# Optimization experiments

Hardware: AMD Instinct MI355X
Metric: run time of the kernel (lower is better)

Reference implementation:

```python
import jax, jax.numpy as jnp
import numpy as np

NUM_GRAPHS = 4
INPUT_SIZE = 50000          # nodes per graph
BOTTLENECK = 64
FFN = 128
HIDDEN = [1, 8, 16]         # hidden_channels; convs go 16->8 then 8->1
E = 3200000                 # num edges (avg degree 16)
N = NUM_GRAPHS * INPUT_SIZE # total nodes = 200000


def setup_inputs() -> dict:
    key = jax.random.key(0)
    ks = jax.random.split(key, 12)
    d = {}
    d["x"] = jax.random.normal(ks[0], (NUM_GRAPHS, BOTTLENECK), dtype=jnp.float32)
    d["edge_index"] = jax.random.randint(ks[1], (2, E), 0, N, dtype=jnp.int64)
    d["edge_weight"] = jax.random.uniform(ks[2], (E,), dtype=jnp.float32)
    # learned params (stored as [in, out] so forward is x @ W + b)
    d["fc1_w"] = jax.random.normal(ks[3], (BOTTLENECK, FFN), dtype=jnp.float32) / np.sqrt(BOTTLENECK)
    d["fc1_b"] = jnp.zeros((FFN,), dtype=jnp.float32)
    d["fc2_w"] = jax.random.normal(ks[4], (FFN, INPUT_SIZE * HIDDEN[-1]), dtype=jnp.float32) / np.sqrt(FFN)
    d["fc2_b"] = jnp.zeros((INPUT_SIZE * HIDDEN[-1],), dtype=jnp.float32)
    d["conv0_w"] = jax.random.normal(ks[5], (HIDDEN[2], HIDDEN[1]), dtype=jnp.float32) / np.sqrt(HIDDEN[2])
    d["conv0_b"] = jnp.zeros((HIDDEN[1],), dtype=jnp.float32)
    d["conv1_w"] = jax.random.normal(ks[6], (HIDDEN[1], HIDDEN[0]), dtype=jnp.float32) / np.sqrt(HIDDEN[1])
    d["conv1_b"] = jnp.zeros((HIDDEN[0],), dtype=jnp.float32)
    d["num_graphs"] = NUM_GRAPHS
    return d


def _gcn_conv(x, row, col, ew, W, b, n_nodes):
    """PyG GCNConv: add self loops (weight 1), symmetric normalization,
    scatter-add of normalized source features, then linear weight + bias."""
    loop = jnp.arange(n_nodes, dtype=row.dtype)
    r = jnp.concatenate([row, loop])
    c = jnp.concatenate([col, loop])
    w = jnp.concatenate([ew, jnp.ones((n_nodes,), dtype=ew.dtype)])
    deg = jax.ops.segment_sum(w, c, num_segments=n_nodes)          # [N]
    dinv = jnp.where(deg > 0, jax.lax.rsqrt(deg), 0.0)
    norm = dinv[r] * w * dinv[c]                                    # [E+N]
    h = x @ W                                                       # [N, out]
    msg = h[r] * norm[:, None]                                      # gather + scale
    out = jax.ops.segment_sum(msg, c, num_segments=n_nodes)        # scatter-add
    return out + b


def reference(x, edge_index, edge_weight, fc1_w, fc1_b, fc2_w, fc2_b,
              conv0_w, conv0_b, conv1_w, conv1_b, num_graphs):
    act = jax.nn.elu
    row, col = edge_index[0], edge_index[1]
    n_nodes = num_graphs * INPUT_SIZE
    z = act(x @ fc1_w + fc1_b)                                     # [G, ffn]
    z = act(z @ fc2_w + fc2_b)                                     # [G, input_size*hidden[-1]]
    h = z.reshape(n_nodes, HIDDEN[-1])                             # [N, 16]
    out = _gcn_conv(h, row, col, edge_weight, conv0_w, conv0_b, n_nodes)  # 16->8
    out = act(out)                                                 # act except last layer
    out = _gcn_conv(out, row, col, edge_weight, conv1_w, conv1_b, n_nodes)  # 8->1
    return out
```

## Files before the change

kernel.cpp:

```cpp
#include <hip/hip_runtime.h>
#include <cstddef>

#define NGRAPH  4
#define NPG     50000
#define NNODES  200000
#define BNECK   64
#define FFN     128
#define COLS    800000
#define NEDGE   3200000
#define H2      16
#define H1      8
#define SCAN_B  512
#define NB      ((NNODES + SCAN_B - 1) / SCAN_B)

__device__ __forceinline__ float elu(float x) {
    return x > 0.f ? x : expm1f(x);
}

__global__ void k_fc1(const float* __restrict__ x, const float* __restrict__ w,
                      const float* __restrict__ b, float* __restrict__ z1) {
    int t = threadIdx.x;
    int g = t >> 7, j = t & 127;
    float acc = b[j];
    #pragma unroll 8
    for (int i = 0; i < BNECK; ++i)
        acc = fmaf(x[g * BNECK + i], w[i * FFN + j], acc);
    z1[t] = elu(acc);
}

__global__ void k_zero(int* __restrict__ p, int n) {
    int i = blockIdx.x * blockDim.x + threadIdx.x;
    if (i < n) p[i] = 0;
}

__global__ void k_hist(const int* __restrict__ col, int* __restrict__ cnt) {
    int e = blockIdx.x * blockDim.x + threadIdx.x;
    if (e < NEDGE) atomicAdd(&cnt[col[e]], 1);
}

__global__ void k_bsum(const int* __restrict__ cnt, int* __restrict__ bsum) {
    __shared__ int s[SCAN_B];
    int t = threadIdx.x;
    int i = blockIdx.x * SCAN_B + t;
    s[t] = (i < NNODES) ? cnt[i] : 0;
    __syncthreads();
    for (int st = SCAN_B / 2; st > 0; st >>= 1) {
        if (t < st) s[t] += s[t + st];
        __syncthreads();
    }
    if (t == 0) bsum[blockIdx.x] = s[0];
}

__global__ void k_btop(const int* __restrict__ bsum, int* __restrict__ bstart) {
    __shared__ int s[SCAN_B];
    int t = threadIdx.x;
    int v = (t < NB) ? bsum[t] : 0;
    s[t] = v;
    __syncthreads();
    for (int st = 1; st < SCAN_B; st <<= 1) {
        int x = (t >= st) ? s[t - st] : 0;
        __syncthreads();
        s[t] += x;
        __syncthreads();
    }
    if (t < NB) bstart[t] = s[t] - v;
}

__global__ void k_bscan(int* __restrict__ cnt, const int* __restrict__ bstart) {
    __shared__ int s[SCAN_B];
    int t = threadIdx.x;
    int i = blockIdx.x * SCAN_B + t;
    int v = (i < NNODES) ? cnt[i] : 0;
    s[t] = v;
    __syncthreads();
    for (int st = 1; st < SCAN_B; st <<= 1) {
        int x = (t >= st) ? s[t - st] : 0;
        __syncthreads();
        s[t] += x;
        __syncthreads();
    }
    if (i < NNODES) cnt[i] = bstart[blockIdx.x] + s[t] - v;
}

__global__ void k_place(const int* __restrict__ row, const int* __restrict__ col,
                        const float* __restrict__ ew,
                        int* __restrict__ offs, int2* __restrict__ csr) {
    int e = blockIdx.x * blockDim.x + threadIdx.x;
    if (e >= NEDGE) return;
    int c = col[e];
    int pos = atomicAdd(&offs[c], 1);
    int2 ent;
    ent.x = row[e];
    ent.y = __float_as_int(ew[e]);
    csr[pos] = ent;
}

__global__ void k_deg(const int* __restrict__ offs, const int2* __restrict__ csr,
                      float* __restrict__ dinv) {
    int n = blockIdx.x * blockDim.x + threadIdx.x;
    if (n >= NNODES) return;
    int s0 = n ? offs[n - 1] : 0;
    int e0 = offs[n];
    float d = 1.0f;
    for (int j = s0; j < e0; ++j) d += __int_as_float(csr[j].y);
    dinv[n] = rsqrtf(d);
}

__global__ __launch_bounds__(256) void k_fc2(
    const float* __restrict__ z1, const float* __restrict__ w2,
    const float* __restrict__ b2, const float* __restrict__ cw0,
    const float* __restrict__ dinv,
    float* __restrict__ hws, float* __restrict__ acc0)
{
    __shared__ float s_z1[NGRAPH * FFN];
    __shared__ float s_cw[H2 * H1];
    __shared__ float s_h[NGRAPH][1024];

    int t = threadIdx.x;
    for (int i = t; i < NGRAPH * FFN; i += 256) s_z1[i] = z1[i];
    if (t < H2 * H1) s_cw[t] = cw0[t];
    __syncthreads();

    int j0 = blockIdx.x * 1024;
    int jj = j0 + t * 4;
    if (jj < COLS) {
        float4 a0 = {0,0,0,0}, a1 = {0,0,0,0}, a2 = {0,0,0,0}, a3 = {0,0,0,0};
        #pragma unroll 4
        for (int i = 0; i < FFN; ++i) {
            const float4 wv = *reinterpret_cast<const float4*>(&w2[(size_t)i * COLS + jj]);
            float zg0 = s_z1[0 * FFN + i];
            float zg1 = s_z1[1 * FFN + i];
            float zg2 = s_z1[2 * FFN + i];
            float zg3 = s_z1[3 * FFN + i];
            a0.x = fmaf(zg0, wv.x, a0.x); a0.y = fmaf(zg0, wv.y, a0.y);
            a0.z = fmaf(zg0, wv.z, a0.z); a0.w = fmaf(zg0, wv.w, a0.w);
            a1.x = fmaf(zg1, wv.x, a1.x); a1.y = fmaf(zg1, wv.y, a1.y);
            a1.z = fmaf(zg1, wv.z, a1.z); a1.w = fmaf(zg1, wv.w, a1.w);
            a2.x = fmaf(zg2, wv.x, a2.x); a2.y = fmaf(zg2, wv.y, a2.y);
            a2.z = fmaf(zg2, wv.z, a2.z); a2.w = fmaf(zg2, wv.w, a2.w);
            a3.x = fmaf(zg3, wv.x, a3.x); a3.y = fmaf(zg3, wv.y, a3.y);
            a3.z = fmaf(zg3, wv.z, a3.z); a3.w = fmaf(zg3, wv.w, a3.w);
        }
        const float4 bv = *reinterpret_cast<const float4*>(&b2[jj]);
        s_h[0][t*4+0] = elu(a0.x + bv.x); s_h[0][t*4+1] = elu(a0.y + bv.y);
        s_h[0][t*4+2] = elu(a0.z + bv.z); s_h[0][t*4+3] = elu(a0.w + bv.w);
        s_h[1][t*4+0] = elu(a1.x + bv.x); s_h[1][t*4+1] = elu(a1.y + bv.y);
        s_h[1][t*4+2] = elu(a1.z + bv.z); s_h[1][t*4+3] = elu(a1.w + bv.w);
        s_h[2][t*4+0] = elu(a2.x + bv.x); s_h[2][t*4+1] = elu(a2.y + bv.y);
        s_h[2][t*4+2] = elu(a2.z + bv.z); s_h[2][t*4+3] = elu(a2.w + bv.w);
        s_h[3][t*4+0] = elu(a3.x + bv.x); s_h[3][t*4+1] = elu(a3.y + bv.y);
        s_h[3][t*4+2] = elu(a3.z + bv.z); s_h[3][t*4+3] = elu(a3.w + bv.w);
    }
    __syncthreads();

    int nbase = j0 >> 4;
    for (int o = t; o < NGRAPH * 64 * H1; o += 256) {
        int g  = o >> 9;
        int lo = o & 511;
        int nl = lo >> 3;
        int m  = lo & 7;
        int nloc = nbase + nl;
        if (nloc < NPG) {
            const float* hr = &s_h[g][nl * 16];
            float s = 0.f;
            #pragma unroll
            for (int k = 0; k < H2; ++k) s = fmaf(hr[k], s_cw[k * H1 + m], s);
            int node = g * NPG + nloc;
            float di = dinv[node];
            hws[node * H1 + m]  = s * di;
            acc0[node * H1 + m] = s * (di * di);
        }
    }
}

__global__ void k_gather0(const int* __restrict__ offs, const int2* __restrict__ csr,
                          const float* __restrict__ hws, const float* __restrict__ acc0,
                          const float* __restrict__ b0, const float* __restrict__ cw1,
                          const float* __restrict__ dinv, float* __restrict__ h1s) {
    int n = blockIdx.x * blockDim.x + threadIdx.x;
    if (n >= NNODES) return;
    int s0 = n ? offs[n - 1] : 0;
    int e0 = offs[n];
    float4 mA = {0,0,0,0}, mB = {0,0,0,0};
    for (int j = s0; j < e0; ++j) {
        int2 ent = csr[j];
        int   r = ent.x;
        float w = __int_as_float(ent.y);
        const float4 ha = *reinterpret_cast<const float4*>(&hws[r * H1]);
        const float4 hb = *reinterpret_cast<const float4*>(&hws[r * H1 + 4]);
        mA.x = fmaf(ha.x, w, mA.x); mA.y = fmaf(ha.y, w, mA.y);
        mA.z = fmaf(ha.z, w, mA.z); mA.w = fmaf(ha.w, w, mA.w);
        mB.x = fmaf(hb.x, w, mB.x); mB.y = fmaf(hb.y, w, mB.y);
        mB.z = fmaf(hb.z, w, mB.z); mB.w = fmaf(hb.w, w, mB.w);
    }
    float dc = dinv[n];
    const float4 sA = *reinterpret_cast<const float4*>(&acc0[n * H1]);
    const float4 sB = *reinterpret_cast<const float4*>(&acc0[n * H1 + 4]);
    float s = 0.f;
    s = fmaf(elu(sA.x + dc * mA.x + b0[0]), cw1[0], s);
    s = fmaf(elu(sA.y + dc * mA.y + b0[1]), cw1[1], s);
    s = fmaf(elu(sA.z + dc * mA.z + b0[2]), cw1[2], s);
    s = fmaf(elu(sA.w + dc * mA.w + b0[3]), cw1[3], s);
    s = fmaf(elu(sB.x + dc * mB.x + b0[4]), cw1[4], s);
    s = fmaf(elu(sB.y + dc * mB.y + b0[5]), cw1[5], s);
    s = fmaf(elu(sB.z + dc * mB.z + b0[6]), cw1[6], s);
    s = fmaf(elu(sB.w + dc * mB.w + b0[7]), cw1[7], s);
    h1s[n] = s * dc;
}

__global__ void k_gather1(const int* __restrict__ offs, const int2* __restrict__ csr,
                          const float* __restrict__ h1s, const float* __restrict__ dinv,
                          const float* __restrict__ cb1, float* __restrict__ out) {
    int n = blockIdx.x * blockDim.x + threadIdx.x;
    if (n >= NNODES) return;
    int s0 = n ? offs[n - 1] : 0;
    int e0 = offs[n];
    float a = h1s[n];
    for (int j = s0; j < e0; ++j) {
        int2 ent = csr[j];
        a = fmaf(h1s[ent.x], __int_as_float(ent.y), a);
    }
    out[n] = cb1[0] + a * dinv[n];
}

extern "C" void kernel_launch(void* const* d_in, const int* in_sizes, int n_in,
                              void* d_out, int out_size, void* d_ws, size_t ws_size,
                              hipStream_t stream) {
    const float* x    = (const float*)d_in[0];
    const int*   ei   = (const int*)d_in[1];
    const float* ew   = (const float*)d_in[2];
    const float* fc1w = (const float*)d_in[3];
    const float* fc1b = (const float*)d_in[4];
    const float* fc2w = (const float*)d_in[5];
    const float* fc2b = (const float*)d_in[6];
    const float* cw0  = (const float*)d_in[7];
    const float* cb0  = (const float*)d_in[8];
    const float* cw1  = (const float*)d_in[9];
    const float* cb1  = (const float*)d_in[10];
    float* out = (float*)d_out;

    float* ws    = (float*)d_ws;
    float* z1    = ws;
    float* dinv  = ws + 512;
    float* hws   = dinv + NNODES;
    float* acc0  = hws + (size_t)NNODES * H1;
    float* h1s   = acc0 + (size_t)NNODES * H1;
    int*   offs  = (int*)(h1s + NNODES);
    int*   bsum  = offs + NNODES;
    int*   bst   = bsum + SCAN_B;
    int2*  csr   = (int2*)(bst + SCAN_B);

    const int* row = ei;
    const int* col = ei + NEDGE;

    k_fc1 <<<1, 512, 0, stream>>>(x, fc1w, fc1b, z1);
    k_zero<<<(NNODES + 255) / 256, 256, 0, stream>>>(offs, NNODES);
    k_hist<<<(NEDGE + 255) / 256, 256, 0, stream>>>(col, offs);
    k_bsum<<<NB, SCAN_B, 0, stream>>>(offs, bsum);
    k_btop<<<1, SCAN_B, 0, stream>>>(bsum, bst);
    k_bscan<<<NB, SCAN_B, 0, stream>>>(offs, bst);
    k_place<<<(NEDGE + 255) / 256, 256, 0, stream>>>(row, col, ew, offs, csr);
    k_deg<<<(NNODES + 255) / 256, 256, 0, stream>>>(offs, csr, dinv);
    k_fc2<<<(COLS + 1023) / 1024, 256, 0, stream>>>(z1, fc2w, fc2b, cw0, dinv, hws, acc0);
    k_gather0<<<(NNODES + 255) / 256, 256, 0, stream>>>(offs, csr, hws, acc0, cb0, cw1, dinv, h1s);
    k_gather1<<<(NNODES + 255) / 256, 256, 0, stream>>>(offs, csr, h1s, dinv, cb1, out);
}
```

Baseline: 1.101 ms.

## Build padded ELL adjacency with overflow list instead of CSR via scan

Replaces the histogram + three-kernel prefix scan + CSR placement with a single ELL placement kernel that writes each edge into a fixed-width (40) per-node slot, spilling rare high-degree edges into a small overflow list. Placement blocks are partitioned by destination range to localize atomics, at the cost of rereading the edge list multiple times. Degree and both gather kernels are rewritten for the ELL layout with a linear scan of the overflow list for spilled nodes. The path is selected only if the workspace is large enough; otherwise the old CSR path is used.

```diff
diff --git a/kernel.cpp b/kernel.cpp
--- a/kernel.cpp
+++ b/kernel.cpp
@@ -10,6 +10,14 @@
 #define NEDGE   3200000
 #define H2      16
 #define H1      8
+
+#define MAXDEG  40
+#define OVCAP   8192
+#define RANGES  16
+#define RW      (NNODES / RANGES)
+#define EPB     4096
+#define CH      ((NEDGE + EPB - 1) / EPB)
+
 #define SCAN_B  512
 #define NB      ((NNODES + SCAN_B - 1) / SCAN_B)
 
@@ -33,77 +41,56 @@
     if (i < n) p[i] = 0;
 }
 
-__global__ void k_hist(const int* __restrict__ col, int* __restrict__ cnt) {
-    int e = blockIdx.x * blockDim.x + threadIdx.x;
-    if (e < NEDGE) atomicAdd(&cnt[col[e]], 1);
-}
-
-__global__ void k_bsum(const int* __restrict__ cnt, int* __restrict__ bsum) {
-    __shared__ int s[SCAN_B];
-    int t = threadIdx.x;
-    int i = blockIdx.x * SCAN_B + t;
-    s[t] = (i < NNODES) ? cnt[i] : 0;
-    __syncthreads();
-    for (int st = SCAN_B / 2; st > 0; st >>= 1) {
-        if (t < st) s[t] += s[t + st];
-        __syncthreads();
-    }
-    if (t == 0) bsum[blockIdx.x] = s[0];
-}
-
-__global__ void k_btop(const int* __restrict__ bsum, int* __restrict__ bstart) {
-    __shared__ int s[SCAN_B];
-    int t = threadIdx.x;
-    int v = (t < NB) ? bsum[t] : 0;
-    s[t] = v;
-    __syncthreads();
-    for (int st = 1; st < SCAN_B; st <<= 1) {
-        int x = (t >= st) ? s[t - st] : 0;
-        __syncthreads();
-        s[t] += x;
-        __syncthreads();
-    }
-    if (t < NB) bstart[t] = s[t] - v;
-}
-
-__global__ void k_bscan(int* __restrict__ cnt, const int* __restrict__ bstart) {
-    __shared__ int s[SCAN_B];
-    int t = threadIdx.x;
-    int i = blockIdx.x * SCAN_B + t;
-    int v = (i < NNODES) ? cnt[i] : 0;
-    s[t] = v;
-    __syncthreads();
-    for (int st = 1; st < SCAN_B; st <<= 1) {
-        int x = (t >= st) ? s[t - st] : 0;
-        __syncthreads();
-        s[t] += x;
-        __syncthreads();
-    }
-    if (i < NNODES) cnt[i] = bstart[blockIdx.x] + s[t] - v;
-}
-
-__global__ void k_place(const int* __restrict__ row, const int* __restrict__ col,
-                        const float* __restrict__ ew,
-                        int* __restrict__ offs, int2* __restrict__ csr) {
-    int e = blockIdx.x * blockDim.x + threadIdx.x;
-    if (e >= NEDGE) return;
-    int c = col[e];
-    int pos = atomicAdd(&offs[c], 1);
-    int2 ent;
-    ent.x = row[e];
-    ent.y = __float_as_int(ew[e]);
-    csr[pos] = ent;
-}
-
-__global__ void k_deg(const int* __restrict__ offs, const int2* __restrict__ csr,
-                      float* __restrict__ dinv) {
-    int n = blockIdx.x * blockDim.x + threadIdx.x;
-    if (n >= NNODES) return;
-    int s0 = n ? offs[n - 1] : 0;
-    int e0 = offs[n];
-    float d = 1.0f;
-    for (int j = s0; j < e0; ++j) d += __int_as_float(csr[j].y);
-    dinv[n] = rsqrtf(d);
+__global__ void k_place_ell(const int* __restrict__ row, const int* __restrict__ col,
+                            const float* __restrict__ ew,
+                            int* __restrict__ cnt, int2* __restrict__ ell,
+                            int* __restrict__ ovc, int3* __restrict__ ovf) {
+    int b = blockIdx.x;
+    int x = b & 7;
+    int q = b >> 3;
+    int p = q / CH;
+    int chunk = q - p * CH;
+    int c0 = (p * 8 + x) * RW;
+    int c1 = c0 + RW;
+    int base = chunk * EPB;
+    #pragma unroll
+    for (int i = 0; i < EPB / 256; ++i) {
+        int e = base + i * 256 + threadIdx.x;
+        if (e < NEDGE) {
+            int c = col[e];
+            if (c >= c0 && c < c1) {
+                int pos = atomicAdd(&cnt[c], 1);
+                if (pos < MAXDEG) {
+                    int2 ent; ent.x = row[e]; ent.y = __float_as_int(ew[e]);
+                    ell[(size_t)c * MAXDEG + pos] = ent;
+                } else {
+                    int o = atomicAdd(ovc, 1);
+                    if (o < OVCAP) {
+                        int3 ent3; ent3.x = c; ent3.y = row[e]; ent3.z = __float_as_int(ew[e]);
+                        ovf[o] = ent3;
+                    }
+                }
+            }
+        }
+    }
+}
+
+__global__ void k_deg_ell(const int* __restrict__ cnt, const int2* __restrict__ ell,
+                          const int* __restrict__ ovc, const int3* __restrict__ ovf,
+                          float* __restrict__ dinv) {
+    int n = blockIdx.x * blockDim.x + threadIdx.x;
+    if (n >= NNODES) return;
+    int d = cnt[n];
+    int m = d < MAXDEG ? d : MAXDEG;
+    const int2* en = &ell[(size_t)n * MAXDEG];
+    float s = 1.0f;
+    for (int j = 0; j < m; ++j) s += __int_as_float(en[j].y);
+    if (d > MAXDEG) {
+        int oc = *ovc; if (oc > OVCAP) oc = OVCAP;
+        for (int j = 0; j < oc; ++j)
+            if (ovf[j].x == n) s += __int_as_float(ovf[j].z);
+    }
+    dinv[n] = rsqrtf(s);
 }
 
 __global__ __launch_bounds__(256) void k_fc2(
@@ -173,6 +160,152 @@
     }
 }
 
+__global__ void k_gather0_ell(const int* __restrict__ cnt, const int2* __restrict__ ell,
+                              const int* __restrict__ ovc, const int3* __restrict__ ovf,
+                              const float* __restrict__ hws, const float* __restrict__ acc0,
+                              const float* __restrict__ b0, const float* __restrict__ cw1,
+                              const float* __restrict__ dinv, float* __restrict__ h1s) {
+    int n = blockIdx.x * blockDim.x + threadIdx.x;
+    if (n >= NNODES) return;
+    int d = cnt[n];
+    int m = d < MAXDEG ? d : MAXDEG;
+    const int2* en = &ell[(size_t)n * MAXDEG];
+    float4 mA = {0,0,0,0}, mB = {0,0,0,0};
+    for (int j = 0; j < m; ++j) {
+        int2 ent = en[j];
+        float w = __int_as_float(ent.y);
+        const float4 ha = *reinterpret_cast<const float4*>(&hws[ent.x * H1]);
+        const float4 hb = *reinterpret_cast<const float4*>(&hws[ent.x * H1 + 4]);
+        mA.x = fmaf(ha.x, w, mA.x); mA.y = fmaf(ha.y, w, mA.y);
+        mA.z = fmaf(ha.z, w, mA.z); mA.w = fmaf(ha.w, w, mA.w);
+        mB.x = fmaf(hb.x, w, mB.x); mB.y = fmaf(hb.y, w, mB.y);
+        mB.z = fmaf(hb.z, w, mB.z); mB.w = fmaf(hb.w, w, mB.w);
+    }
+    if (d > MAXDEG) {
+        int oc = *ovc; if (oc > OVCAP) oc = OVCAP;
+        for (int j = 0; j < oc; ++j) {
+            if (ovf[j].x == n) {
+                float w = __int_as_float(ovf[j].z);
+                int r = ovf[j].y;
+                const float4 ha = *reinterpret_cast<const float4*>(&hws[r * H1]);
+                const float4 hb = *reinterpret_cast<const float4*>(&hws[r * H1 + 4]);
+                mA.x = fmaf(ha.x, w, mA.x); mA.y = fmaf(ha.y, w, mA.y);
+                mA.z = fmaf(ha.z, w, mA.z); mA.w = fmaf(ha.w, w, mA.w);
+                mB.x = fmaf(hb.x, w, mB.x); mB.y = fmaf(hb.y, w, mB.y);
+                mB.z = fmaf(hb.z, w, mB.z); mB.w = fmaf(hb.w, w, mB.w);
+            }
+        }
+    }
+    float dc = dinv[n];
+    const float4 sA = *reinterpret_cast<const float4*>(&acc0[n * H1]);
+    const float4 sB = *reinterpret_cast<const float4*>(&acc0[n * H1 + 4]);
+    float s = 0.f;
+    s = fmaf(elu(sA.x + dc * mA.x + b0[0]), cw1[0], s);
+    s = fmaf(elu(sA.y + dc * mA.y + b0[1]), cw1[1], s);
+    s = fmaf(elu(sA.z + dc * mA.z + b0[2]), cw1[2], s);
+    s = fmaf(elu(sA.w + dc * mA.w + b0[3]), cw1[3], s);
+    s = fmaf(elu(sB.x + dc * mB.x + b0[4]), cw1[4], s);
+    s = fmaf(elu(sB.y + dc * mB.y + b0[5]), cw1[5], s);
+    s = fmaf(elu(sB.z + dc * mB.z + b0[6]), cw1[6], s);
+    s = fmaf(elu(sB.w + dc * mB.w + b0[7]), cw1[7], s);
+    h1s[n] = s * dc;
+}
+
+__global__ void k_gather1_ell(const int* __restrict__ cnt, const int2* __restrict__ ell,
+                              const int* __restrict__ ovc, const int3* __restrict__ ovf,
+                              const float* __restrict__ h1s, const float* __restrict__ dinv,
+                              const float* __restrict__ cb1, float* __restrict__ out) {
+    int n = blockIdx.x * blockDim.x + threadIdx.x;
+    if (n >= NNODES) return;
+    int d = cnt[n];
+    int m = d < MAXDEG ? d : MAXDEG;
+    const int2* en = &ell[(size_t)n * MAXDEG];
+    float a = h1s[n];
+    for (int j = 0; j < m; ++j) {
+        int2 ent = en[j];
+        a = fmaf(h1s[ent.x], __int_as_float(ent.y), a);
+    }
+    if (d > MAXDEG) {
+        int oc = *ovc; if (oc > OVCAP) oc = OVCAP;
+        for (int j = 0; j < oc; ++j)
+            if (ovf[j].x == n) a = fmaf(h1s[ovf[j].y], __int_as_float(ovf[j].z), a);
+    }
+    out[n] = cb1[0] + a * dinv[n];
+}
+
+__global__ void k_hist(const int* __restrict__ col, int* __restrict__ cnt) {
+    int e = blockIdx.x * blockDim.x + threadIdx.x;
+    if (e < NEDGE) atomicAdd(&cnt[col[e]], 1);
+}
+
+__global__ void k_bsum(const int* __restrict__ cnt, int* __restrict__ bsum) {
+    __shared__ int s[SCAN_B];
+    int t = threadIdx.x;
+    int i = blockIdx.x * SCAN_B + t;
+    s[t] = (i < NNODES) ? cnt[i] : 0;
+    __syncthreads();
+    for (int st = SCAN_B / 2; st > 0; st >>= 1) {
+        if (t < st) s[t] += s[t + st];
+        __syncthreads();
+    }
+    if (t == 0) bsum[blockIdx.x] = s[0];
+}
+
+__global__ void k_btop(const int* __restrict__ bsum, int* __restrict__ bstart) {
+    __shared__ int s[SCAN_B];
+    int t = threadIdx.x;
+    int v = (t < NB) ? bsum[t] : 0;
+    s[t] = v;
+    __syncthreads();
+    for (int st = 1; st < SCAN_B; st <<= 1) {
+        int x = (t >= st) ? s[t - st] : 0;
+        __syncthreads();
+        s[t] += x;
+        __syncthreads();
+    }
+    if (t < NB) bstart[t] = s[t] - v;
+}
+
+__global__ void k_bscan(int* __restrict__ cnt, const int* __restrict__ bstart) {
+    __shared__ int s[SCAN_B];
+    int t = threadIdx.x;
+    int i = blockIdx.x * SCAN_B + t;
+    int v = (i < NNODES) ? cnt[i] : 0;
+    s[t] = v;
+    __syncthreads();
+    for (int st = 1; st < SCAN_B; st <<= 1) {
+        int x = (t >= st) ? s[t - st] : 0;
+        __syncthreads();
+        s[t] += x;
+        __syncthreads();
+    }
+    if (i < NNODES) cnt[i] = bstart[blockIdx.x] + s[t] - v;
+}
+
+__global__ void k_place(const int* __restrict__ row, const int* __restrict__ col,
+                        const float* __restrict__ ew,
+                        int* __restrict__ offs, int2* __restrict__ csr) {
+    int e = blockIdx.x * blockDim.x + threadIdx.x;
+    if (e >= NEDGE) return;
+    int c = col[e];
+    int pos = atomicAdd(&offs[c], 1);
+    int2 ent;
+    ent.x = row[e];
+    ent.y = __float_as_int(ew[e]);
+    csr[pos] = ent;
+}
+
+__global__ void k_deg(const int* __restrict__ offs, const int2* __restrict__ csr,
+                      float* __restrict__ dinv) {
+    int n = blockIdx.x * blockDim.x + threadIdx.x;
+    if (n >= NNODES) return;
+    int s0 = n ? offs[n - 1] : 0;
+    int e0 = offs[n];
+    float d = 1.0f;
+    for (int j = s0; j < e0; ++j) d += __int_as_float(csr[j].y);
+    dinv[n] = rsqrtf(d);
+}
+
 __global__ void k_gather0(const int* __restrict__ offs, const int2* __restrict__ csr,
                           const float* __restrict__ hws, const float* __restrict__ acc0,
                           const float* __restrict__ b0, const float* __restrict__ cw1,
@@ -239,29 +372,51 @@
     const float* cb1  = (const float*)d_in[10];
     float* out = (float*)d_out;
 
+    const int* row = ei;
+    const int* col = ei + NEDGE;
+
     float* ws    = (float*)d_ws;
     float* z1    = ws;
     float* dinv  = ws + 512;
     float* hws   = dinv + NNODES;
     float* acc0  = hws + (size_t)NNODES * H1;
     float* h1s   = acc0 + (size_t)NNODES * H1;
-    int*   offs  = (int*)(h1s + NNODES);
-    int*   bsum  = offs + NNODES;
-    int*   bst   = bsum + SCAN_B;
-    int2*  csr   = (int2*)(bst + SCAN_B);
-
-    const int* row = ei;
-    const int* col = ei + NEDGE;
-
-    k_fc1 <<<1, 512, 0, stream>>>(x, fc1w, fc1b, z1);
-    k_zero<<<(NNODES + 255) / 256, 256, 0, stream>>>(offs, NNODES);
-    k_hist<<<(NEDGE + 255) / 256, 256, 0, stream>>>(col, offs);
-    k_bsum<<<NB, SCAN_B, 0, stream>>>(offs, bsum);
-    k_btop<<<1, SCAN_B, 0, stream>>>(bsum, bst);
-    k_bscan<<<NB, SCAN_B, 0, stream>>>(offs, bst);
-    k_place<<<(NEDGE + 255) / 256, 256, 0, stream>>>(row, col, ew, offs, csr);
-    k_deg<<<(NNODES + 255) / 256, 256, 0, stream>>>(offs, csr, dinv);
-    k_fc2<<<(COLS + 1023) / 1024, 256, 0, stream>>>(z1, fc2w, fc2b, cw0, dinv, hws, acc0);
-    k_gather0<<<(NNODES + 255) / 256, 256, 0, stream>>>(offs, csr, hws, acc0, cb0, cw1, dinv, h1s);
-    k_gather1<<<(NNODES + 255) / 256, 256, 0, stream>>>(offs, csr, h1s, dinv, cb1, out);
-}
+
+    size_t ell_units = 512 + NNODES + 2u * (size_t)NNODES * H1 + NNODES
+                     + (NNODES + 8) + (3u * OVCAP) + 2u * (size_t)NNODES * MAXDEG;
+    bool use_ell = ws_size >= ell_units * 4u + 256u;
+
+    if (use_ell) {
+        int*  cnt = (int*)(h1s + NNODES);
+        int*  ovc = cnt + NNODES;
+        int3* ovf = (int3*)(ovc + 8);
+        int2* ell = (int2*)((int*)ovf + 3 * OVCAP);
+
+        k_fc1 <<<1, 512, 0, stream>>>(x, fc1w, fc1b, z1);
+        k_zero<<<(NNODES + 8 + 255) / 256, 256, 0, stream>>>(cnt, NNODES + 8);
+        k_place_ell<<<2 * CH * 8, 256, 0, stream>>>(row, col, ew, cnt, ell, ovc, ovf);
+        k_deg_ell<<<(NNODES + 255) / 256, 256, 0, stream>>>(cnt, ell, ovc, ovf, dinv);
+        k_fc2<<<(COLS + 1023) / 1024, 256, 0, stream>>>(z1, fc2w, fc2b, cw0, dinv, hws, acc0);
+        k_gather0_ell<<<(NNODES + 255) / 256, 256, 0, stream>>>(cnt, ell, ovc, ovf, hws, acc0,
+                                                                cb0, cw1, dinv, h1s);
+        k_gather1_ell<<<(NNODES + 255) / 256, 256, 0, stream>>>(cnt, ell, ovc, ovf, h1s, dinv,
+                                                                cb1, out);
+    } else {
+        int*   offs  = (int*)(h1s + NNODES);
+        int*   bsum  = offs + NNODES;
+        int*   bst   = bsum + SCAN_B;
+        int2*  csr   = (int2*)(bst + SCAN_B);
+
+        k_fc1 <<<1, 512, 0, stream>>>(x, fc1w, fc1b, z1);
+        k_zero<<<(NNODES + 255) / 256, 256, 0, stream>>>(offs, NNODES);
+        k_hist<<<(NEDGE + 255) / 256, 256, 0, stream>>>(col, offs);
+        k_bsum<<<NB, SCAN_B, 0, stream>>>(offs, bsum);
+        k_btop<<<1, SCAN_B, 0, stream>>>(bsum, bst);
+        k_bscan<<<NB, SCAN_B, 0, stream>>>(offs, bst);
+        k_place<<<(NEDGE + 255) / 256, 256, 0, stream>>>(row, col, ew, offs, csr);
+        k_deg<<<(NNODES + 255) / 256, 256, 0, stream>>>(offs, csr, dinv);
+        k_fc2<<<(COLS + 1023) / 1024, 256, 0, stream>>>(z1, fc2w, fc2b, cw0, dinv, hws, acc0);
+        k_gather0<<<(NNODES + 255) / 256, 256, 0, stream>>>(offs, csr, hws, acc0, cb0, cw1, dinv, h1s);
+        k_gather1<<<(NNODES + 255) / 256, 256, 0, stream>>>(offs, csr, h1s, dinv, cb1, out);
+    }
+}
```

New measurement: 952.1 us. 13.5% less time.
